# Kernel tuning notes

Hardware: AMD Instinct MI355X
Metric: run time of the kernel (lower is better)

## Reference

```python
import jax, jax.numpy as jnp
import numpy as np

H, HKV, DH, T_MAX = 32, 8, 128, 4096
ROPE_BASE = 500000.0


def apply_rope(x, pos, base):
    # x: [B, h, T, D]; MLX rope, traditional=False (split-half rotation)
    B, h, T, D = x.shape
    half = D // 2
    inv_freq = 1.0 / (base ** (jnp.arange(half, dtype=jnp.float32) * 2.0 / D))
    t = (pos + jnp.arange(T)).astype(jnp.float32)  # absolute positions
    ang = t[:, None] * inv_freq[None, :]           # [T, half]
    cos = jnp.cos(ang)[None, None]                 # [1,1,T,half]
    sin = jnp.sin(ang)[None, None]
    x1, x2 = x[..., :half], x[..., half:]
    return jnp.concatenate([x1 * cos - x2 * sin, x2 * cos + x1 * sin], axis=-1)


def setup_inputs() -> dict:
    key = jax.random.key(0)
    ks = jax.random.split(key, 5)
    hidden = 4096
    return {
        "hidden_states": jax.random.normal(ks[0], (1, 2048, hidden), jnp.float32),
        "Wq": jax.random.normal(ks[1], (hidden, H * DH), jnp.float32) * 0.02,
        "Wk": jax.random.normal(ks[2], (hidden, HKV * DH), jnp.float32) * 0.02,
        "Wv": jax.random.normal(ks[3], (hidden, HKV * DH), jnp.float32) * 0.02,
        "Wo": jax.random.normal(ks[4], (H * DH, hidden), jnp.float32) * 0.02,
        "pos_int": 0,
    }


def reference(hidden_states, Wq, Wk, Wv, Wo, pos_int):
    B, T, _ = hidden_states.shape
    q = (hidden_states @ Wq).reshape(B, T, H, DH).transpose(0, 2, 1, 3)    # [B,H,T,D]
    k = (hidden_states @ Wk).reshape(B, T, HKV, DH).transpose(0, 2, 1, 3)  # [B,Hkv,T,D]
    v = (hidden_states @ Wv).reshape(B, T, HKV, DH).transpose(0, 2, 1, 3)

    q = apply_rope(q, pos_int, ROPE_BASE)
    k = apply_rope(k, pos_int, ROPE_BASE)

    # KV cache: write at [pos:pos+T], then slice [:pos+T] (pos is static Python int)
    k_cache = jnp.zeros((B, HKV, T_MAX, DH), jnp.float32)
    v_cache = jnp.zeros((B, HKV, T_MAX, DH), jnp.float32)
    k_cache = jax.lax.dynamic_update_slice(k_cache, k, (0, 0, pos_int, 0))
    v_cache = jax.lax.dynamic_update_slice(v_cache, v, (0, 0, pos_int, 0))
    end_pos = pos_int + T
    k_ = k_cache[:, :, :end_pos, :]  # [B,Hkv,S,D]
    v_ = v_cache[:, :, :end_pos, :]
    S = end_pos

    # GQA without materializing repeat_interleave: group query heads per kv head
    group = H // HKV
    qg = q.reshape(B, HKV, group, T, DH)
    scale = 1.0 / jnp.sqrt(jnp.float32(DH))
    scores = jnp.einsum("bhgtd,bhsd->bhgts", qg, k_) * scale  # [B,Hkv,g,T,S]
    # torch SDPA is_causal=True: top-left aligned mask (allow s <= t)
    causal = jnp.arange(S)[None, :] <= jnp.arange(T)[:, None]  # [T,S]
    scores = jnp.where(causal[None, None, None], scores, -jnp.inf)
    probs = jax.nn.softmax(scores, axis=-1)
    attn = jnp.einsum("bhgts,bhsd->bhgtd", probs, v_)          # [B,Hkv,g,T,D]
    attn = attn.reshape(B, H, T, DH).transpose(0, 2, 1, 3).reshape(B, T, H * DH)
    return attn @ Wo
```

## Files before the change

### kernel.cpp

```cpp
#include <hip/hip_runtime.h>
#include <hip/hip_bf16.h>
#include <math.h>

typedef unsigned short u16;
typedef __attribute__((ext_vector_type(4))) float f32x4;
typedef __attribute__((ext_vector_type(8))) short bf16x8;

#define GLD16(gptr, lptr) __builtin_amdgcn_global_load_lds( \
    (const __attribute__((address_space(1))) void*)(gptr),  \
    (__attribute__((address_space(3))) void*)(lptr), 16, 0, 0)

__device__ __forceinline__ float bf2f(u16 u) {
  union { unsigned int i; float f; } c; c.i = ((unsigned int)u) << 16; return c.f;
}
__device__ __forceinline__ u16 f2bf(float f) {
  union { float f; unsigned int i; } c; c.f = f;
  unsigned int r = c.i + 0x7fffu + ((c.i >> 16) & 1u);
  return (u16)(r >> 16);
}

__global__ __launch_bounds__(256) void f32_to_bf16(const float* __restrict__ in,
                                                   u16* __restrict__ out, int n4) {
  int i = blockIdx.x * 256 + threadIdx.x;
  if (i >= n4) return;
  float4 v = reinterpret_cast<const float4*>(in)[i];
  ushort4 o;
  o.x = f2bf(v.x); o.y = f2bf(v.y); o.z = f2bf(v.z); o.w = f2bf(v.w);
  reinterpret_cast<ushort4*>(out)[i] = o;
}

__global__ __launch_bounds__(256) void transpose_convert(const float* __restrict__ W,
                                                         u16* __restrict__ Wt,
                                                         int K, int N) {
  __shared__ float tile[32][33];
  const int n0 = blockIdx.x * 32, k0 = blockIdx.y * 32;
  const int tx = threadIdx.x & 31, ty = threadIdx.x >> 5;
#pragma unroll
  for (int r = 0; r < 32; r += 8)
    tile[ty + r][tx] = W[(size_t)(k0 + ty + r) * N + (n0 + tx)];
  __syncthreads();
#pragma unroll
  for (int r = 0; r < 32; r += 8)
    Wt[(size_t)(n0 + ty + r) * K + (k0 + tx)] = f2bf(tile[tx][ty + r]);
}

__global__ __launch_bounds__(256) void transpose_v(const u16* __restrict__ Vsrc,
                                                   u16* __restrict__ Vt) {
  __shared__ u16 tile[32][33];
  const int t0 = blockIdx.x * 32, d0 = blockIdx.y * 32, hkv = blockIdx.z;
  const int tx = threadIdx.x & 31, ty = threadIdx.x >> 5;
#pragma unroll
  for (int r = 0; r < 32; r += 8)
    tile[ty + r][tx] = Vsrc[(size_t)(t0 + ty + r) * 6144 + hkv * 128 + d0 + tx];
  __syncthreads();
#pragma unroll
  for (int r = 0; r < 32; r += 8)
    Vt[((size_t)hkv * 128 + d0 + ty + r) * 2048 + t0 + tx] = tile[tx][ty + r];
}

__global__ __launch_bounds__(256) void rope_table(float2* __restrict__ tab,
                                                  const int* __restrict__ pos_ptr) {
  int idx = blockIdx.x * 256 + threadIdx.x;
  int d = idx & 63, t = idx >> 6;
  int pos = *pos_ptr;
  float inv = exp2f(-(float)d * (0.015625f * 18.931568569324174f));
  float ang = (float)(pos + t) * inv;
  tab[idx] = make_float2(cosf(ang), sinf(ang));
}

__global__ __launch_bounds__(256) void rope_apply(u16* __restrict__ X, int nheads,
                                                  int stride,
                                                  const float2* __restrict__ tab) {
  int idx = blockIdx.x * 256 + threadIdx.x;
  int total = 2048 * nheads * 64;
  if (idx >= total) return;
  int d = idx & 63;
  int h = (idx >> 6) % nheads;
  int t = idx / (64 * nheads);
  float2 cs = tab[t * 64 + d];
  size_t base = (size_t)t * stride + h * 128 + d;
  float x1 = bf2f(X[base]);
  float x2 = bf2f(X[base + 64]);
  X[base]      = f2bf(x1 * cs.x - x2 * cs.y);
  X[base + 64] = f2bf(x2 * cs.x + x1 * cs.y);
}

template <int OUT_BF16>
__global__ __launch_bounds__(512, 2) void gemm_big(const u16* __restrict__ A,
                                                   const u16* __restrict__ Bt,
                                                   void* __restrict__ C,
                                                   int M, int N, int K,
                                                   int ntiles, size_t zstride) {
  __shared__ alignas(16) u16 As[2][256 * 64];
  __shared__ alignas(16) u16 Bs[2][256 * 64];
  const int tid = threadIdx.x;
  const int lane = tid & 63, wid = tid >> 6;
  const int l15 = lane & 15, lg = lane >> 4;
  const int wm = wid >> 2, wn = wid & 3;
  const int wvb = tid & ~63;
  const int z = blockIdx.z;
  const int ko = z * ntiles * 64;

  const int nwg = gridDim.x * gridDim.y;
  const int id0 = blockIdx.y * gridDim.x + blockIdx.x;
  const int id = (id0 & 7) * (nwg >> 3) + (id0 >> 3);
  const int n0 = (id % gridDim.x) * 256;
  const int m0 = (id / gridDim.x) * 256;

  f32x4 acc[8][4];
#pragma unroll
  for (int i = 0; i < 8; ++i)
#pragma unroll
    for (int j = 0; j < 4; ++j) {
      f32x4 zz = {0.f, 0.f, 0.f, 0.f};
      acc[i][j] = zz;
    }

#define STAGE(s_, b_)                                                           \
  do {                                                                          \
    _Pragma("unroll")                                                           \
    for (int p = 0; p < 4; ++p) {                                               \
      const int slot = p * 512 + tid;                                           \
      const int row = slot >> 3, ch = slot & 7;                                 \
      const int col = (ch ^ (row & 7)) * 8;                                     \
      GLD16(A + (size_t)(m0 + row) * K + ko + (s_) * 64 + col,                  \
            &As[b_][(p * 512 + wvb) * 8]);                                      \
      GLD16(Bt + (size_t)(n0 + row) * K + ko + (s_) * 64 + col,                 \
            &Bs[b_][(p * 512 + wvb) * 8]);                                      \
    }                                                                           \
  } while (0)

  STAGE(0, 0);
  __syncthreads();
  int cur = 0;

  for (int t = 0; t < ntiles; ++t) {
    if (t + 1 < ntiles) STAGE(t + 1, cur ^ 1);
#pragma unroll
    for (int g = 0; g < 2; ++g) {
      bf16x8 af[8], bfr[4];
#pragma unroll
      for (int i = 0; i < 8; ++i) {
        const int row = wm * 128 + i * 16 + l15;
        const int ch = (g * 4 + lg) ^ (row & 7);
        af[i] = *reinterpret_cast<const bf16x8*>(&As[cur][row * 64 + ch * 8]);
      }
#pragma unroll
      for (int j = 0; j < 4; ++j) {
        const int row = wn * 64 + j * 16 + l15;
        const int ch = (g * 4 + lg) ^ (row & 7);
        bfr[j] = *reinterpret_cast<const bf16x8*>(&Bs[cur][row * 64 + ch * 8]);
      }
      __builtin_amdgcn_s_setprio(1);
#pragma unroll
      for (int i = 0; i < 8; ++i)
#pragma unroll
        for (int j = 0; j < 4; ++j)
          acc[i][j] = __builtin_amdgcn_mfma_f32_16x16x32_bf16(af[i], bfr[j], acc[i][j], 0, 0, 0);
      __builtin_amdgcn_s_setprio(0);
    }
    __syncthreads();
    cur ^= 1;
  }
#undef STAGE

  u16* Cb = (u16*)C + (size_t)z * zstride;
#pragma unroll
  for (int i = 0; i < 8; ++i)
#pragma unroll
    for (int j = 0; j < 4; ++j)
#pragma unroll
      for (int r = 0; r < 4; ++r) {
        const int row = m0 + wm * 128 + i * 16 + lg * 4 + r;
        const int col = n0 + wn * 64 + j * 16 + l15;
        const float v = acc[i][j][r];
        if (OUT_BF16) Cb[(size_t)row * N + col] = f2bf(v);
        else          ((float*)C)[(size_t)row * N + col] = v;
      }
}

__global__ __launch_bounds__(256) void wo_reduce(const u16* __restrict__ P,
                                                 float* __restrict__ out) {
  const size_t i = ((size_t)blockIdx.x * 256 + threadIdx.x) * 8;
  bf16x8 a = *reinterpret_cast<const bf16x8*>(P + i);
  bf16x8 b = *reinterpret_cast<const bf16x8*>(P + 8388608 + i);
  float4 o0, o1;
  o0.x = bf2f((u16)a[0]) + bf2f((u16)b[0]);
  o0.y = bf2f((u16)a[1]) + bf2f((u16)b[1]);
  o0.z = bf2f((u16)a[2]) + bf2f((u16)b[2]);
  o0.w = bf2f((u16)a[3]) + bf2f((u16)b[3]);
  o1.x = bf2f((u16)a[4]) + bf2f((u16)b[4]);
  o1.y = bf2f((u16)a[5]) + bf2f((u16)b[5]);
  o1.z = bf2f((u16)a[6]) + bf2f((u16)b[6]);
  o1.w = bf2f((u16)a[7]) + bf2f((u16)b[7]);
  *reinterpret_cast<float4*>(out + i) = o0;
  *reinterpret_cast<float4*>(out + i + 4) = o1;
}

__global__ __launch_bounds__(512) void attn_kernel(const u16* __restrict__ Q,
                                                   const u16* __restrict__ K,
                                                   const u16* __restrict__ Vt,
                                                   u16* __restrict__ O,
                                                   const int* __restrict__ pos_ptr) {
  const int pos = *pos_ptr;
  const int h = blockIdx.y;
  const int hkv = h >> 2;
  const int tid = threadIdx.x;
  const int w = tid >> 6, lane = tid & 63;
  const int l15 = lane & 15, lg = lane >> 4;

  __shared__ alignas(16) u16 Ks[2][64 * 128];
  __shared__ alignas(16) u16 Vs[2][128 * 64];
  __shared__ alignas(16) u16 Pl[8][16][72];

  const u16* Kh = K + hkv * 128;
  const u16* Vh = Vt + (size_t)hkv * 128 * 2048;

  const float C = 0.12752961957823275f;
  const float THR = 62.0f;
  const int wvb = tid & ~63;

#define STAGE_TILE(st_, b_)                                                        \
  do {                                                                             \
    const int s0_ = (st_) * 64;                                                    \
    _Pragma("unroll")                                                              \
    for (int p = 0; p < 2; ++p) {                                                  \
      const int idx = p * 512 + tid;                                               \
      const int kr = idx >> 4, kc = (idx & 15) ^ (kr & 7);                         \
      GLD16(Kh + (size_t)(s0_ + kr) * 6144 + kc * 8, &Ks[b_][(p * 512 + wvb) * 8]);\
      const int vr = idx >> 3, vc = (idx & 7) ^ (vr & 7);                          \
      GLD16(Vh + (size_t)vr * 2048 + s0_ + vc * 8, &Vs[b_][(p * 512 + wvb) * 8]);  \
    }                                                                              \
  } while (0)

  for (int pass = 0; pass < 2; ++pass) {
    const int qb = (pass == 0) ? (8 + (int)blockIdx.x) : (7 - (int)blockIdx.x);
    const int qt0 = qb * 128;
    const int nst = 2 * qb + 2;
    const int frag_base = qt0 + w * 16;

    bf16x8 qa[4];
#pragma unroll
    for (int kk = 0; kk < 4; ++kk)
      qa[kk] = *reinterpret_cast<const bf16x8*>(
          Q + (size_t)(frag_base + l15) * 6144 + h * 128 + kk * 32 + lg * 8);

    f32x4 acc[8];
#pragma unroll
    for (int i = 0; i < 8; ++i) { f32x4 z = {0.f, 0.f, 0.f, 0.f}; acc[i] = z; }
    float mrun[4], lpart[4];
#pragma unroll
    for (int r = 0; r < 4; ++r) {
      mrun[r] = (pos > 0) ? 0.0f : -INFINITY;
      lpart[r] = 0.0f;
    }

    STAGE_TILE(0, 0);
    __syncthreads();
    int cur = 0;

    for (int st = 0; st < nst; ++st) {
      if (st + 1 < nst) STAGE_TILE(st + 1, cur ^ 1);
      const int s0 = st * 64;

      float pv[4][4];
      __builtin_amdgcn_s_setprio(1);
#pragma unroll
      for (int sub = 0; sub < 4; ++sub) {
        f32x4 s4 = {0.f, 0.f, 0.f, 0.f};
        const int row = sub * 16 + l15;
#pragma unroll
        for (int kk = 0; kk < 4; ++kk) {
          const int chunk = (kk * 4 + lg) ^ (row & 7);
          bf16x8 kf = *reinterpret_cast<const bf16x8*>(&Ks[cur][row * 128 + chunk * 8]);
          s4 = __builtin_amdgcn_mfma_f32_16x16x32_bf16(qa[kk], kf, s4, 0, 0, 0);
        }
#pragma unroll
        for (int r = 0; r < 4; ++r) pv[sub][r] = s4[r];
      }
      __builtin_amdgcn_s_setprio(0);

      if (s0 + 64 > frag_base) {
#pragma unroll
        for (int r = 0; r < 4; ++r) {
          const int qrow = frag_base + lg * 4 + r;
#pragma unroll
          for (int sub = 0; sub < 4; ++sub) {
            const int scol = s0 + sub * 16 + l15;
            pv[sub][r] = (scol <= qrow) ? pv[sub][r] : -INFINITY;
          }
        }
      }

      float lmax[4];
#pragma unroll
      for (int r = 0; r < 4; ++r)
        lmax[r] = fmaxf(fmaxf(pv[0][r], pv[1][r]), fmaxf(pv[2][r], pv[3][r]));
      float dml = fmaxf(fmaxf(lmax[0] - mrun[0], lmax[1] - mrun[1]),
                        fmaxf(lmax[2] - mrun[2], lmax[3] - mrun[3]));
      if (!__all(dml <= THR)) {
        float sfr[4];
#pragma unroll
        for (int r = 0; r < 4; ++r) {
          float mx = lmax[r];
#pragma unroll
          for (int off = 1; off < 16; off <<= 1) mx = fmaxf(mx, __shfl_xor(mx, off));
          const float mnew = fmaxf(mrun[r], mx);
          sfr[r] = exp2f((mrun[r] - mnew) * C);
          mrun[r] = mnew;
          lpart[r] *= sfr[r];
        }
#pragma unroll
        for (int dc = 0; dc < 8; ++dc)
#pragma unroll
          for (int r = 0; r < 4; ++r) acc[dc][r] *= sfr[r];
      }

#pragma unroll
      for (int r = 0; r < 4; ++r) {
        const float nmC = -mrun[r] * C;
        float ps = 0.0f;
#pragma unroll
        for (int sub = 0; sub < 4; ++sub) {
          const float p = exp2f(fmaf(pv[sub][r], C, nmC));
          pv[sub][r] = p;
          ps += p;
        }
        lpart[r] += ps;
      }

#pragma unroll
      for (int sub = 0; sub < 4; ++sub)
#pragma unroll
        for (int r = 0; r < 4; ++r)
          Pl[w][lg * 4 + r][sub * 16 + l15] = f2bf(pv[sub][r]);

      __builtin_amdgcn_s_setprio(1);
#pragma unroll
      for (int ks = 0; ks < 2; ++ks) {
        bf16x8 pf = *reinterpret_cast<const bf16x8*>(&Pl[w][l15][ks * 32 + lg * 8]);
#pragma unroll
        for (int dc = 0; dc < 8; ++dc) {
          const int row = dc * 16 + l15;
          const int chunk = (ks * 4 + lg) ^ (row & 7);
          bf16x8 vf = *reinterpret_cast<const bf16x8*>(&Vs[cur][row * 64 + chunk * 8]);
          acc[dc] = __builtin_amdgcn_mfma_f32_16x16x32_bf16(pf, vf, acc[dc], 0, 0, 0);
        }
      }
      __builtin_amdgcn_s_setprio(0);

      __syncthreads();
      cur ^= 1;
    }

#pragma unroll
    for (int r = 0; r < 4; ++r) {
      float l = lpart[r];
#pragma unroll
      for (int off = 1; off < 16; off <<= 1) l += __shfl_xor(l, off);
      if (pos > 0) l += (float)pos * exp2f(-mrun[r] * C);
      const float linv = 1.0f / l;
      const int qrow = frag_base + lg * 4 + r;
#pragma unroll
      for (int dc = 0; dc < 8; ++dc)
        O[(size_t)qrow * 4096 + h * 128 + dc * 16 + l15] = f2bf(acc[dc][r] * linv);
    }
  }
#undef STAGE_TILE
}

extern "C" void kernel_launch(void* const* d_in, const int* in_sizes, int n_in,
                              void* d_out, int out_size, void* d_ws, size_t ws_size,
                              hipStream_t stream) {
  const float* hs = (const float*)d_in[0];
  const float* Wq = (const float*)d_in[1];
  const float* Wk = (const float*)d_in[2];
  const float* Wv = (const float*)d_in[3];
  const float* Wo = (const float*)d_in[4];
  const int* pos  = (const int*)d_in[5];

  char* ws = (char*)d_ws;
  u16* hs_bf = (u16*)(ws + 0);
  u16* WT    = (u16*)(ws + 16777216ULL);
  u16* QKVb  = (u16*)(ws + 67108864ULL);
  u16* attnO = hs_bf;
  u16* WoT   = WT;
  u16* Vtg   = (u16*)(ws + 50331648ULL);
  float2* tabF = (float2*)(ws + 54525952ULL);
  u16* Ppart = (u16*)(ws + 50331648ULL);

  f32_to_bf16<<<8192, 256, 0, stream>>>(hs, hs_bf, 2097152);
  transpose_convert<<<dim3(128, 128), 256, 0, stream>>>(Wq, WT, 4096, 4096);
  transpose_convert<<<dim3(32, 128), 256, 0, stream>>>(Wk, WT + (size_t)4096 * 4096, 4096, 1024);
  transpose_convert<<<dim3(32, 128), 256, 0, stream>>>(Wv, WT + (size_t)5120 * 4096, 4096, 1024);

  gemm_big<1><<<dim3(24, 8, 1), 512, 0, stream>>>(hs_bf, WT, QKVb, 2048, 6144, 4096, 64, 0);

  transpose_convert<<<dim3(128, 128), 256, 0, stream>>>(Wo, WoT, 4096, 4096);

  rope_table<<<512, 256, 0, stream>>>(tabF, pos);
  rope_apply<<<16384, 256, 0, stream>>>(QKVb, 32, 6144, tabF);
  rope_apply<<<4096, 256, 0, stream>>>(QKVb + 4096, 8, 6144, tabF);

  transpose_v<<<dim3(64, 4, 8), 256, 0, stream>>>(QKVb + 5120, Vtg);

  attn_kernel<<<dim3(8, 32), 512, 0, stream>>>(QKVb, QKVb + 4096, Vtg, attnO, pos);

  gemm_big<1><<<dim3(16, 8, 2), 512, 0, stream>>>(attnO, WoT, Ppart, 2048, 4096, 4096,
                                                  32, 8388608);
  wo_reduce<<<4096, 256, 0, stream>>>(Ppart, (float*)d_out);
}
```

Measured before the change: 373.2 us.

## Add 4-stage pipelined BK=32 GEMM with XCD-aware tile remap for QKV projection

```diff
diff --git a/kernel.cpp b/kernel.cpp
--- a/kernel.cpp
+++ b/kernel.cpp
@@ -83,6 +83,138 @@
   float x2 = bf2f(X[base + 64]);
   X[base]      = f2bf(x1 * cs.x - x2 * cs.y);
   X[base + 64] = f2bf(x2 * cs.x + x1 * cs.y);
+}
+
+template <int OUT_BF16>
+__global__ __launch_bounds__(512, 2) void gemm_pipe(const u16* __restrict__ A,
+                                                    const u16* __restrict__ Bt,
+                                                    void* __restrict__ C,
+                                                    int M, int N, int K) {
+  __shared__ alignas(16) u16 As[4][256 * 32];
+  __shared__ alignas(16) u16 Bs[4][256 * 32];
+  const int tid = threadIdx.x;
+  const int lane = tid & 63, wid = tid >> 6;
+  const int l15 = lane & 15, lg = lane >> 4;
+  const int wm = wid >> 2, wn = wid & 3;
+  const int wvb = tid & ~63;
+
+  const int nwg = gridDim.x * gridDim.y;
+  const int id0 = blockIdx.y * gridDim.x + blockIdx.x;
+  const int id = (id0 & 7) * (nwg >> 3) + (id0 >> 3);
+  const int n0 = (id % gridDim.x) * 256;
+  const int m0 = (id / gridDim.x) * 256;
+
+  f32x4 acc[8][4];
+#pragma unroll
+  for (int i = 0; i < 8; ++i)
+#pragma unroll
+    for (int j = 0; j < 4; ++j) {
+      f32x4 z = {0.f, 0.f, 0.f, 0.f};
+      acc[i][j] = z;
+    }
+
+#define SWZ4(row_) (((row_) ^ ((row_) >> 2)) & 3)
+#define STAGE_A(s_)                                                             \
+  do {                                                                          \
+    const int b_ = (s_) & 3;                                                    \
+    _Pragma("unroll")                                                           \
+    for (int p = 0; p < 2; ++p) {                                               \
+      const int slot = p * 512 + tid;                                           \
+      const int row = slot >> 2, ch = slot & 3;                                 \
+      const int col = (ch ^ SWZ4(row)) * 8;                                     \
+      GLD16(A + (size_t)(m0 + row) * K + (s_) * 32 + col,                       \
+            &As[b_][(p * 512 + wvb) * 8]);                                      \
+    }                                                                           \
+  } while (0)
+#define STAGE_B(s_)                                                             \
+  do {                                                                          \
+    const int b_ = (s_) & 3;                                                    \
+    _Pragma("unroll")                                                           \
+    for (int p = 0; p < 2; ++p) {                                               \
+      const int slot = p * 512 + tid;                                           \
+      const int row = slot >> 2, ch = slot & 3;                                 \
+      const int col = (ch ^ SWZ4(row)) * 8;                                     \
+      GLD16(Bt + (size_t)(n0 + row) * K + (s_) * 32 + col,                      \
+            &Bs[b_][(p * 512 + wvb) * 8]);                                      \
+    }                                                                           \
+  } while (0)
+
+  const int nt = K >> 5;
+  STAGE_A(0); STAGE_B(0);
+  STAGE_A(1); STAGE_B(1);
+  asm volatile("s_waitcnt vmcnt(4)" ::: "memory");
+  __builtin_amdgcn_s_barrier();
+  asm volatile("" ::: "memory");
+
+  for (int t = 0; t < nt; ++t) {
+    const int b = t & 3;
+    const bool pre = (t + 2 < nt);
+    bf16x8 bfr[4];
+    if (pre) STAGE_A(t + 2);
+    {
+      bf16x8 af[4];
+#pragma unroll
+      for (int i = 0; i < 4; ++i) {
+        const int row = wm * 128 + i * 16 + l15;
+        const int ch = lg ^ SWZ4(row);
+        af[i] = *reinterpret_cast<const bf16x8*>(&As[b][row * 32 + ch * 8]);
+      }
+#pragma unroll
+      for (int j = 0; j < 4; ++j) {
+        const int row = wn * 64 + j * 16 + l15;
+        const int ch = lg ^ SWZ4(row);
+        bfr[j] = *reinterpret_cast<const bf16x8*>(&Bs[b][row * 32 + ch * 8]);
+      }
+      __builtin_amdgcn_s_setprio(1);
+#pragma unroll
+      for (int i = 0; i < 4; ++i)
+#pragma unroll
+        for (int j = 0; j < 4; ++j)
+          acc[i][j] = __builtin_amdgcn_mfma_f32_16x16x32_bf16(af[i], bfr[j], acc[i][j], 0, 0, 0);
+      __builtin_amdgcn_s_setprio(0);
+    }
+    __builtin_amdgcn_s_barrier();
+    asm volatile("" ::: "memory");
+    if (pre) STAGE_B(t + 2);
+    {
+      bf16x8 af[4];
+#pragma unroll
+      for (int i = 0; i < 4; ++i) {
+        const int row = wm * 128 + (4 + i) * 16 + l15;
+        const int ch = lg ^ SWZ4(row);
+        af[i] = *reinterpret_cast<const bf16x8*>(&As[b][row * 32 + ch * 8]);
+      }
+      __builtin_amdgcn_s_setprio(1);
+#pragma unroll
+      for (int i = 0; i < 4; ++i)
+#pragma unroll
+        for (int j = 0; j < 4; ++j)
+          acc[4 + i][j] = __builtin_amdgcn_mfma_f32_16x16x32_bf16(af[i], bfr[j], acc[4 + i][j], 0, 0, 0);
+      __builtin_amdgcn_s_setprio(0);
+    }
+    if (t + 1 < nt) {
+      if (pre) asm volatile("s_waitcnt vmcnt(4)" ::: "memory");
+      else     asm volatile("s_waitcnt vmcnt(0)" ::: "memory");
+      __builtin_amdgcn_s_barrier();
+      asm volatile("" ::: "memory");
+    }
+  }
+#undef STAGE_A
+#undef STAGE_B
+#undef SWZ4
+
+#pragma unroll
+  for (int i = 0; i < 8; ++i)
+#pragma unroll
+    for (int j = 0; j < 4; ++j)
+#pragma unroll
+      for (int r = 0; r < 4; ++r) {
+        const int row = m0 + wm * 128 + i * 16 + lg * 4 + r;
+        const int col = n0 + wn * 64 + j * 16 + l15;
+        const float v = acc[i][j][r];
+        if (OUT_BF16) ((u16*)C)[(size_t)row * N + col] = f2bf(v);
+        else          ((float*)C)[(size_t)row * N + col] = v;
+      }
 }
 
 template <int OUT_BF16>
@@ -394,7 +526,7 @@
   transpose_convert<<<dim3(32, 128), 256, 0, stream>>>(Wk, WT + (size_t)4096 * 4096, 4096, 1024);
   transpose_convert<<<dim3(32, 128), 256, 0, stream>>>(Wv, WT + (size_t)5120 * 4096, 4096, 1024);
 
-  gemm_big<1><<<dim3(24, 8, 1), 512, 0, stream>>>(hs_bf, WT, QKVb, 2048, 6144, 4096, 64, 0);
+  gemm_pipe<1><<<dim3(24, 8), 512, 0, stream>>>(hs_bf, WT, QKVb, 2048, 6144, 4096);
 
   transpose_convert<<<dim3(128, 128), 256, 0, stream>>>(Wo, WoT, 4096, 4096);
 
```

Result: slower. 401.0 us (+7.5%).
